# Kernel optimization log

Measured on AMD Instinct MI355X. Metric: run time of the kernel, lower is better.

The kernel has to match this reference:

```python
import jax, jax.numpy as jnp
import numpy as np

GAMMA = 0.01      # rbf gamma (init kwarg)
C = 10            # n_classes (len(nv))
NV = 500          # support vectors per class (equal segments)
# all (i, j) class pairs with i < j, in the original nested-loop order
PAIRS = np.array([(i, j) for i in range(C) for j in range(i + 1, C)], dtype=np.int32)
I_IDX = jnp.asarray(PAIRS[:, 0])  # [45]
J_IDX = jnp.asarray(PAIRS[:, 1])  # [45]


def setup_inputs() -> dict:
    key = jax.random.key(0)
    k1, k2, k3, k4 = jax.random.split(key, 4)
    x = jax.random.normal(k1, (8192, 256), dtype=jnp.float32)
    sv = jax.random.normal(k2, (5000, 256), dtype=jnp.float32)
    a = jax.random.normal(k3, (C - 1, 5000), dtype=jnp.float32) * 0.1  # dual coefs
    b = jax.random.normal(k4, (45,), dtype=jnp.float32) * 0.1          # intercepts per pair
    return {"x": x, "sv": sv, "a": a, "b": b}


def reference(x, sv, a, b):
    # RBF kernel matrix: k[n, s] = exp(-gamma * ||x_n - sv_s||^2)
    x_norm = jnp.sum(x * x, axis=1)[:, None]            # [N, 1]
    sv_norm = jnp.sum(sv * sv, axis=1)[None, :]         # [1, SV]
    k = jnp.exp(-GAMMA * (x_norm + sv_norm) + 2.0 * GAMMA * (x @ sv.T))  # [N, SV]

    N = x.shape[0]
    kr = k.reshape(N, C, NV)           # per-class SV segments
    ar = a.reshape(C - 1, C, NV)       # dual coef rows, segmented the same way
    # T[n, r, c] = sum_m a[r, segment c, m] * k[n, segment c, m]
    # (fuses every inner Python loop of the original into one contraction)
    T = jnp.einsum('ncm,rcm->nrc', kr, ar)              # [N, C-1, C]

    # decision for pair (i, j): a[i, seg j] . k_seg_j + a[j-1, seg i] . k_seg_i + b
    c = T[:, I_IDX, J_IDX] + T[:, J_IDX - 1, I_IDX] + b[None, :]  # [N, 45]

    # pairwise voting: winner i if c > 0 else j; class id = mode of votes
    votes = jnp.where(c > 0, I_IDX[None, :], J_IDX[None, :])      # [N, 45] int32
    counts = jnp.sum(jax.nn.one_hot(votes, C, dtype=jnp.float32), axis=1)  # [N, C]
    # argmax picks the smallest class index on ties, matching torch.mode
    class_ids = jnp.argmax(counts, axis=1).astype(jnp.int32)
    return (class_ids, class_ids)
```

## Files before the change

kernel.cpp:

```cpp
#include <hip/hip_runtime.h>
#include <hip/hip_fp16.h>
#include <cmath>


#define GAMMA 0.01f
constexpr int N  = 8192;
constexpr int D  = 256;
constexpr int S  = 5000;
constexpr int C  = 10;
constexpr int NV = 500;
constexpr int R  = 9;

typedef _Float16 f16x8 __attribute__((ext_vector_type(8)));
typedef _Float16 f16x4 __attribute__((ext_vector_type(4)));
typedef float    f32x4 __attribute__((ext_vector_type(4)));

__global__ __launch_bounds__(256) void prep_kernel(const float* __restrict__ x,
                                                   const float* __restrict__ sv,
                                                   _Float16* __restrict__ xh,
                                                   _Float16* __restrict__ xl,
                                                   _Float16* __restrict__ sh,
                                                   _Float16* __restrict__ sl,
                                                   float* __restrict__ xn,
                                                   float* __restrict__ svn) {
    int gid  = blockIdx.x * blockDim.x + threadIdx.x;
    int wid  = gid >> 6;
    int lane = gid & 63;
    if (wid >= N + S) return;
    bool isx = wid < N;
    int  r   = isx ? wid : wid - N;
    const float* row = isx ? (x + (size_t)r * D) : (sv + (size_t)r * D);
    float4 v = reinterpret_cast<const float4*>(row)[lane];
    float s = v.x * v.x + v.y * v.y + v.z * v.z + v.w * v.w;
#pragma unroll
    for (int off = 32; off > 0; off >>= 1) s += __shfl_xor(s, off, 64);
    float vv[4] = {v.x, v.y, v.z, v.w};
    f16x4 h, l;
#pragma unroll
    for (int k = 0; k < 4; ++k) {
        _Float16 hi = (_Float16)vv[k];
        h[k] = hi;
        l[k] = (_Float16)((vv[k] - (float)hi) * 4096.0f);
    }
    size_t o = (size_t)r * D + lane * 4;
    *(f16x4*)((isx ? xh : sh) + o) = h;
    *(f16x4*)((isx ? xl : sl) + o) = l;
    if (lane == 0) (isx ? xn : svn)[r] = s;
}

__global__ __launch_bounds__(256, 2) void svc_gemm(const _Float16* __restrict__ xh,
                                                   const _Float16* __restrict__ xl,
                                                   const _Float16* __restrict__ sh,
                                                   const _Float16* __restrict__ sl,
                                                   const float* __restrict__ a,
                                                   const float* __restrict__ xnorm,
                                                   const float* __restrict__ svnorm,
                                                   float* __restrict__ T) {
    __shared__ _Float16 As[2][2][64 * 32];
    __shared__ _Float16 Bs[2][2][128 * 32];
    __shared__ float a_sh[R][512];
    __shared__ float sn_sh[512];
    __shared__ float tred[64 * R];

    const int tid  = threadIdx.x;
    const int n0   = blockIdx.x * 64;
    const int cls  = blockIdx.y;
    const int w    = tid >> 6;
    const int lane = tid & 63;
    const int wm   = w >> 1;
    const int wn   = w & 1;
    const int lx   = lane & 15;
    const int quad = lane >> 4;

    for (int i = tid; i < R * 512; i += 256) {
        int r = i >> 9, cseg = i & 511;
        a_sh[r][cseg] = (cseg < NV) ? a[(size_t)r * S + cls * NV + cseg] : 0.0f;
    }
    for (int i = tid; i < 512; i += 256) {
        int svi = cls * NV + ((i < NV) ? i : NV - 1);
        sn_sh[i] = svnorm[svi];
    }
    for (int i = tid; i < 64 * R; i += 256) tred[i] = 0.0f;

    float xnr[2][4];
#pragma unroll
    for (int ti = 0; ti < 2; ++ti)
#pragma unroll
        for (int reg = 0; reg < 4; ++reg)
            xnr[ti][reg] = xnorm[n0 + wm * 32 + ti * 16 + quad * 4 + reg];

    float tloc[8][R];
#pragma unroll
    for (int i = 0; i < 8; ++i)
#pragma unroll
        for (int r = 0; r < R; ++r) tloc[i][r] = 0.0f;

    int aoff[2], boff[4];
#pragma unroll
    for (int ti = 0; ti < 2; ++ti) {
        int row = wm * 32 + ti * 16 + lx;
        aoff[ti] = row * 32 + ((quad + row) & 3) * 8;
    }
#pragma unroll
    for (int tj = 0; tj < 4; ++tj) {
        int row = wn * 64 + tj * 16 + lx;
        boff[tj] = row * 32 + ((quad + row) & 3) * 8;
    }
    const int arow = tid >> 2, ag = tid & 3;
    const int adst = arow * 32 + ((ag + arow) & 3) * 8;
    const int brow0 = tid >> 2, brow1 = (tid >> 2) + 64;
    const int bdst0 = brow0 * 32 + ((ag + brow0) & 3) * 8;
    const int bdst1 = brow1 * 32 + ((ag + brow1) & 3) * 8;
    const int segend = cls * NV + NV - 1;

    f32x4 accM[2][4], accC[2][4];
#pragma unroll
    for (int ti = 0; ti < 2; ++ti)
#pragma unroll
        for (int tj = 0; tj < 4; ++tj) {
            accM[ti][tj] = (f32x4){0.f, 0.f, 0.f, 0.f};
            accC[ti][tj] = (f32x4){0.f, 0.f, 0.f, 0.f};
        }

    f16x8 pAh, pAl, pBh0, pBl0, pBh1, pBl1;
    auto load_phase = [&](int ph) {
        int ch = ph >> 3, kb = ph & 7;
        size_t goA = (size_t)(n0 + arow) * D + kb * 32 + ag * 8;
        pAh = *(const f16x8*)(xh + goA);
        pAl = *(const f16x8*)(xl + goA);
        int svbase = cls * NV + ch * 128;
        int svr = svbase + brow0; if (svr > segend) svr = segend;
        size_t go = (size_t)svr * D + kb * 32 + ag * 8;
        pBh0 = *(const f16x8*)(sh + go);
        pBl0 = *(const f16x8*)(sl + go);
        svr = svbase + brow1; if (svr > segend) svr = segend;
        go = (size_t)svr * D + kb * 32 + ag * 8;
        pBh1 = *(const f16x8*)(sh + go);
        pBl1 = *(const f16x8*)(sl + go);
    };
    auto store_phase = [&](int buf) {
        *(f16x8*)(&As[buf][0][adst])  = pAh;
        *(f16x8*)(&As[buf][1][adst])  = pAl;
        *(f16x8*)(&Bs[buf][0][bdst0]) = pBh0;
        *(f16x8*)(&Bs[buf][1][bdst0]) = pBl0;
        *(f16x8*)(&Bs[buf][0][bdst1]) = pBh1;
        *(f16x8*)(&Bs[buf][1][bdst1]) = pBl1;
    };

    load_phase(0);
    store_phase(0);
    __syncthreads();

    for (int ph = 0; ph < 32; ++ph) {
        const int buf = ph & 1;
        if (ph < 31) load_phase(ph + 1);

        f16x8 Af[2][2], Bf[2][4];
#pragma unroll
        for (int ti = 0; ti < 2; ++ti) {
            Af[0][ti] = *(const f16x8*)(&As[buf][0][aoff[ti]]);
            Af[1][ti] = *(const f16x8*)(&As[buf][1][aoff[ti]]);
        }
#pragma unroll
        for (int tj = 0; tj < 4; ++tj) {
            Bf[0][tj] = *(const f16x8*)(&Bs[buf][0][boff[tj]]);
            Bf[1][tj] = *(const f16x8*)(&Bs[buf][1][boff[tj]]);
        }
#pragma unroll
        for (int ti = 0; ti < 2; ++ti)
#pragma unroll
            for (int tj = 0; tj < 4; ++tj) {
                accM[ti][tj] = __builtin_amdgcn_mfma_f32_16x16x32_f16(
                    Af[0][ti], Bf[0][tj], accM[ti][tj], 0, 0, 0);
                accC[ti][tj] = __builtin_amdgcn_mfma_f32_16x16x32_f16(
                    Af[0][ti], Bf[1][tj], accC[ti][tj], 0, 0, 0);
                accC[ti][tj] = __builtin_amdgcn_mfma_f32_16x16x32_f16(
                    Af[1][ti], Bf[0][tj], accC[ti][tj], 0, 0, 0);
            }

        if (ph < 31) store_phase(buf ^ 1);
        __syncthreads();

        if ((ph & 7) == 7) {
            const int ch = ph >> 3;
#pragma unroll
            for (int tj = 0; tj < 4; ++tj) {
                int cseg = ch * 128 + wn * 64 + tj * 16 + lx;
                float sn = sn_sh[cseg];
                float av[R];
#pragma unroll
                for (int r = 0; r < R; ++r) av[r] = a_sh[r][cseg];
#pragma unroll
                for (int ti = 0; ti < 2; ++ti)
#pragma unroll
                    for (int reg = 0; reg < 4; ++reg) {
                        float dot = accM[ti][tj][reg]
                                  + accC[ti][tj][reg] * (1.0f / 4096.0f);
                        float e  = fmaf(2.0f * GAMMA, dot,
                                        -GAMMA * (xnr[ti][reg] + sn));
                        float kv = __expf(e);
#pragma unroll
                        for (int r = 0; r < R; ++r)
                            tloc[ti * 4 + reg][r] =
                                fmaf(av[r], kv, tloc[ti * 4 + reg][r]);
                    }
            }
#pragma unroll
            for (int ti = 0; ti < 2; ++ti)
#pragma unroll
                for (int tj = 0; tj < 4; ++tj) {
                    accM[ti][tj] = (f32x4){0.f, 0.f, 0.f, 0.f};
                    accC[ti][tj] = (f32x4){0.f, 0.f, 0.f, 0.f};
                }
        }
    }

#pragma unroll
    for (int i = 0; i < 8; ++i)
#pragma unroll
        for (int r = 0; r < R; ++r) {
            float v = tloc[i][r];
            v += __shfl_xor(v, 1, 64);
            v += __shfl_xor(v, 2, 64);
            v += __shfl_xor(v, 4, 64);
            v += __shfl_xor(v, 8, 64);
            tloc[i][r] = v;
        }
    if (lx == 0) {
#pragma unroll
        for (int i = 0; i < 8; ++i) {
            int ti = i >> 2, reg = i & 3;
            int row = wm * 32 + ti * 16 + quad * 4 + reg;
#pragma unroll
            for (int r = 0; r < R; ++r)
                atomicAdd(&tred[row * R + r], tloc[i][r]);
        }
    }
    __syncthreads();
    for (int i = tid; i < 64 * R; i += 256) {
        int row = i / R, r = i - row * R;
        T[(size_t)(n0 + row) * 90 + r * 10 + cls] = tred[i];
    }
}

__global__ __launch_bounds__(256) void vote_kernel(const float* __restrict__ T,
                                                   const float* __restrict__ b,
                                                   int* __restrict__ out) {
    int n = blockIdx.x * blockDim.x + threadIdx.x;
    if (n >= N) return;
    const float* Tn = T + (size_t)n * 90;
    float tv[90];
#pragma unroll
    for (int i = 0; i < 90; ++i) tv[i] = Tn[i];
    int counts[C];
#pragma unroll
    for (int k = 0; k < C; ++k) counts[k] = 0;
    int p = 0;
#pragma unroll
    for (int i = 0; i < C; ++i) {
#pragma unroll
        for (int j = i + 1; j < C; ++j) {
            float c = tv[i * 10 + j] + tv[(j - 1) * 10 + i] + b[p];
            if (c > 0.f) counts[i]++; else counts[j]++;
            ++p;
        }
    }
    int best = 0;
#pragma unroll
    for (int k = 1; k < C; ++k)
        if (counts[k] > counts[best]) best = k;
    out[n]     = best;
    out[N + n] = best;
}

extern "C" void kernel_launch(void* const* d_in, const int* in_sizes, int n_in,
                              void* d_out, int out_size, void* d_ws, size_t ws_size,
                              hipStream_t stream) {
    const float* x  = (const float*)d_in[0];
    const float* sv = (const float*)d_in[1];
    const float* a  = (const float*)d_in[2];
    const float* b  = (const float*)d_in[3];
    int* out = (int*)d_out;

    char* wp = (char*)d_ws;
    _Float16* xh = (_Float16*)wp;  wp += (size_t)N * D * 2;
    _Float16* xl = (_Float16*)wp;  wp += (size_t)N * D * 2;
    _Float16* sh = (_Float16*)wp;  wp += (size_t)S * D * 2;
    _Float16* sl = (_Float16*)wp;  wp += (size_t)S * D * 2;
    float* xnorm  = (float*)wp;    wp += (size_t)N * 4;
    float* svnorm = (float*)wp;    wp += (size_t)S * 4;
    float* T      = (float*)wp;

    {
        int waves = N + S;
        prep_kernel<<<(waves * 64 + 255) / 256, 256, 0, stream>>>(
            x, sv, xh, xl, sh, sl, xnorm, svnorm);
    }
    {
        dim3 grid(N / 64, C);
        svc_gemm<<<grid, 256, 0, stream>>>(xh, xl, sh, sl, a, xnorm, svnorm, T);
    }
    {
        vote_kernel<<<N / 256, 256, 0, stream>>>(T, b, out);
    }
}
```

Baseline: 204.7 us.

## Single-buffer LDS tiles with padded rows and two-sync loop

```diff
diff --git a/kernel.cpp b/kernel.cpp
--- a/kernel.cpp
+++ b/kernel.cpp
@@ -10,6 +10,7 @@
 constexpr int C  = 10;
 constexpr int NV = 500;
 constexpr int R  = 9;
+constexpr int LW = 40;
 
 typedef _Float16 f16x8 __attribute__((ext_vector_type(8)));
 typedef _Float16 f16x4 __attribute__((ext_vector_type(4)));
@@ -56,8 +57,8 @@
                                                    const float* __restrict__ xnorm,
                                                    const float* __restrict__ svnorm,
                                                    float* __restrict__ T) {
-    __shared__ _Float16 As[2][2][64 * 32];
-    __shared__ _Float16 Bs[2][2][128 * 32];
+    __shared__ _Float16 As[2][64 * LW];
+    __shared__ _Float16 Bs[2][128 * LW];
     __shared__ float a_sh[R][512];
     __shared__ float sn_sh[512];
     __shared__ float tred[64 * R];
@@ -99,18 +100,19 @@
 #pragma unroll
     for (int ti = 0; ti < 2; ++ti) {
         int row = wm * 32 + ti * 16 + lx;
-        aoff[ti] = row * 32 + ((quad + row) & 3) * 8;
+        aoff[ti] = row * LW + ((quad + (row >> 3)) & 3) * 8;
     }
 #pragma unroll
     for (int tj = 0; tj < 4; ++tj) {
         int row = wn * 64 + tj * 16 + lx;
-        boff[tj] = row * 32 + ((quad + row) & 3) * 8;
-    }
-    const int arow = tid >> 2, ag = tid & 3;
-    const int adst = arow * 32 + ((ag + arow) & 3) * 8;
-    const int brow0 = tid >> 2, brow1 = (tid >> 2) + 64;
-    const int bdst0 = brow0 * 32 + ((ag + brow0) & 3) * 8;
-    const int bdst1 = brow1 * 32 + ((ag + brow1) & 3) * 8;
+        boff[tj] = row * LW + ((quad + (row >> 3)) & 3) * 8;
+    }
+    const int arow = tid >> 2, aks = tid & 3;
+    const int adst = arow * LW + ((aks + (arow >> 3)) & 3) * 8;
+    const int baseA = (n0 + arow) * D + aks * 8;
+    const int brow = tid >> 1, bks = (tid & 1) * 2;
+    const int bdst0 = brow * LW + ((bks     + (brow >> 3)) & 3) * 8;
+    const int bdst1 = brow * LW + ((bks + 1 + (brow >> 3)) & 3) * 8;
     const int segend = cls * NV + NV - 1;
 
     f32x4 accM[2][4], accC[2][4];
@@ -122,67 +124,58 @@
             accC[ti][tj] = (f32x4){0.f, 0.f, 0.f, 0.f};
         }
 
-    f16x8 pAh, pAl, pBh0, pBl0, pBh1, pBl1;
-    auto load_phase = [&](int ph) {
-        int ch = ph >> 3, kb = ph & 7;
-        size_t goA = (size_t)(n0 + arow) * D + kb * 32 + ag * 8;
-        pAh = *(const f16x8*)(xh + goA);
-        pAl = *(const f16x8*)(xl + goA);
-        int svbase = cls * NV + ch * 128;
-        int svr = svbase + brow0; if (svr > segend) svr = segend;
-        size_t go = (size_t)svr * D + kb * 32 + ag * 8;
-        pBh0 = *(const f16x8*)(sh + go);
-        pBl0 = *(const f16x8*)(sl + go);
-        svr = svbase + brow1; if (svr > segend) svr = segend;
-        go = (size_t)svr * D + kb * 32 + ag * 8;
-        pBh1 = *(const f16x8*)(sh + go);
-        pBl1 = *(const f16x8*)(sl + go);
+    f16x8 pAh, pAl, pBh0, pBh1, pBl0, pBl1;
+    auto loadG = [&](int ch, int kb) {
+        int offA = baseA + kb * 32;
+        pAh = *(const f16x8*)(xh + offA);
+        pAl = *(const f16x8*)(xl + offA);
+        int svr = cls * NV + ch * 128 + brow;
+        if (svr > segend) svr = segend;
+        int offB = svr * D + bks * 8 + kb * 32;
+        pBh0 = *(const f16x8*)(sh + offB);
+        pBh1 = *(const f16x8*)(sh + offB + 8);
+        pBl0 = *(const f16x8*)(sl + offB);
+        pBl1 = *(const f16x8*)(sl + offB + 8);
     };
-    auto store_phase = [&](int buf) {
-        *(f16x8*)(&As[buf][0][adst])  = pAh;
-        *(f16x8*)(&As[buf][1][adst])  = pAl;
-        *(f16x8*)(&Bs[buf][0][bdst0]) = pBh0;
-        *(f16x8*)(&Bs[buf][1][bdst0]) = pBl0;
-        *(f16x8*)(&Bs[buf][0][bdst1]) = pBh1;
-        *(f16x8*)(&Bs[buf][1][bdst1]) = pBl1;
-    };
-
-    load_phase(0);
-    store_phase(0);
+
+    loadG(0, 0);
     __syncthreads();
 
     for (int ph = 0; ph < 32; ++ph) {
-        const int buf = ph & 1;
-        if (ph < 31) load_phase(ph + 1);
-
-        f16x8 Af[2][2], Bf[2][4];
+        const int ch = ph >> 3, kb = ph & 7;
+        *(f16x8*)(&As[0][adst])  = pAh;
+        *(f16x8*)(&As[1][adst])  = pAl;
+        *(f16x8*)(&Bs[0][bdst0]) = pBh0;
+        *(f16x8*)(&Bs[0][bdst1]) = pBh1;
+        *(f16x8*)(&Bs[1][bdst0]) = pBl0;
+        *(f16x8*)(&Bs[1][bdst1]) = pBl1;
+        __syncthreads();
+
+        if (ph < 31) loadG((ph + 1) >> 3, (ph + 1) & 7);
+
+        f16x8 Ah[2], Al[2];
 #pragma unroll
         for (int ti = 0; ti < 2; ++ti) {
-            Af[0][ti] = *(const f16x8*)(&As[buf][0][aoff[ti]]);
-            Af[1][ti] = *(const f16x8*)(&As[buf][1][aoff[ti]]);
+            Ah[ti] = *(const f16x8*)(&As[0][aoff[ti]]);
+            Al[ti] = *(const f16x8*)(&As[1][aoff[ti]]);
         }
 #pragma unroll
         for (int tj = 0; tj < 4; ++tj) {
-            Bf[0][tj] = *(const f16x8*)(&Bs[buf][0][boff[tj]]);
-            Bf[1][tj] = *(const f16x8*)(&Bs[buf][1][boff[tj]]);
-        }
-#pragma unroll
-        for (int ti = 0; ti < 2; ++ti)
-#pragma unroll
-            for (int tj = 0; tj < 4; ++tj) {
+            f16x8 Bh = *(const f16x8*)(&Bs[0][boff[tj]]);
+            f16x8 Bl = *(const f16x8*)(&Bs[1][boff[tj]]);
+#pragma unroll
+            for (int ti = 0; ti < 2; ++ti) {
                 accM[ti][tj] = __builtin_amdgcn_mfma_f32_16x16x32_f16(
-                    Af[0][ti], Bf[0][tj], accM[ti][tj], 0, 0, 0);
+                    Ah[ti], Bh, accM[ti][tj], 0, 0, 0);
                 accC[ti][tj] = __builtin_amdgcn_mfma_f32_16x16x32_f16(
-                    Af[0][ti], Bf[1][tj], accC[ti][tj], 0, 0, 0);
+                    Ah[ti], Bl, accC[ti][tj], 0, 0, 0);
                 accC[ti][tj] = __builtin_amdgcn_mfma_f32_16x16x32_f16(
-                    Af[1][ti], Bf[0][tj], accC[ti][tj], 0, 0, 0);
+                    Al[ti], Bh, accC[ti][tj], 0, 0, 0);
             }
-
-        if (ph < 31) store_phase(buf ^ 1);
+        }
         __syncthreads();
 
-        if ((ph & 7) == 7) {
-            const int ch = ph >> 3;
+        if (kb == 7) {
 #pragma unroll
             for (int tj = 0; tj < 4; ++tj) {
                 int cseg = ch * 128 + wn * 64 + tj * 16 + lx;
```

Measured after the change: 212.9 us. +4.0%, slower.
